# Kernel tuning notes

Hardware: AMD Instinct MI355X
Metric: run time of the kernel (lower is better)

The kernel has to match this reference:

```python
import jax, jax.numpy as jnp
import numpy as np

D = 768        # embed dim
DEPTH = 12     # num blocks
H = 12         # heads
HD = D // H    # head dim = 64
P = 16         # patch size
IMG = 224
NPATCH = (IMG // P) ** 2   # 196
N = NPATCH + 1             # +cls = 197
MLP = 4 * D                # 3072
NC = 100                   # classes
R = 8                      # lora rank
LORA_SCALE = 16.0 / R      # alpha / r = 2.0
EPS = 1e-6                 # timm LayerNorm eps


def setup_inputs() -> dict:
    key = jax.random.key(0)
    ks = jax.random.split(key, 12)
    def g(k, shape, s=0.02):
        return jax.random.normal(k, shape, dtype=jnp.float32) * s
    f32 = jnp.float32
    return {
        "x": jax.random.normal(ks[0], (32, 3, IMG, IMG), dtype=f32),
        "patch_w": g(ks[1], (D, 3, P, P)),
        "patch_b": jnp.zeros((D,), f32),
        "cls_token": g(ks[2], (1, 1, D)),
        "pos_embed": g(ks[3], (1, N, D)),
        "ln1_g": jnp.ones((DEPTH, D), f32),  "ln1_b": jnp.zeros((DEPTH, D), f32),
        "qkv_w": g(ks[4], (DEPTH, 3 * D, D)), "qkv_b": jnp.zeros((DEPTH, 3 * D), f32),
        "lora_A": g(ks[5], (DEPTH, D, R), 0.1), "lora_B": g(ks[6], (DEPTH, R, 3 * D), 0.1),
        "proj_w": g(ks[7], (DEPTH, D, D)), "proj_b": jnp.zeros((DEPTH, D), f32),
        "ln2_g": jnp.ones((DEPTH, D), f32),  "ln2_b": jnp.zeros((DEPTH, D), f32),
        "fc1_w": g(ks[8], (DEPTH, MLP, D)), "fc1_b": jnp.zeros((DEPTH, MLP), f32),
        "fc2_w": g(ks[9], (DEPTH, D, MLP)), "fc2_b": jnp.zeros((DEPTH, D), f32),
        "norm_g": jnp.ones((D,), f32), "norm_b": jnp.zeros((D,), f32),
        "head_w": g(ks[10], (NC, D)), "head_b": jnp.zeros((NC,), f32),
    }


def _ln(x, g, b):
    m = x.mean(-1, keepdims=True)
    v = ((x - m) ** 2).mean(-1, keepdims=True)
    return (x - m) * jax.lax.rsqrt(v + EPS) * g + b


def reference(x, patch_w, patch_b, cls_token, pos_embed,
              ln1_g, ln1_b, qkv_w, qkv_b, lora_A, lora_B, proj_w, proj_b,
              ln2_g, ln2_b, fc1_w, fc1_b, fc2_w, fc2_b,
              norm_g, norm_b, head_w, head_b):
    B = x.shape[0]
    # patch embed: non-overlapping PxP conv == unfold + linear
    xp = x.reshape(B, 3, IMG // P, P, IMG // P, P).transpose(0, 2, 4, 1, 3, 5)
    xp = xp.reshape(B, NPATCH, 3 * P * P)              # [B, 196, 768]
    t = xp @ patch_w.reshape(D, -1).T + patch_b        # [B, 196, D]
    t = jnp.concatenate([jnp.broadcast_to(cls_token, (B, 1, D)), t], axis=1)
    t = t + pos_embed                                   # [B, N, D]

    scale = HD ** -0.5
    for i in range(DEPTH):
        h = _ln(t, ln1_g[i], ln1_b[i])
        # frozen qkv GEMM + LoRA low-rank branch (dropout = identity at eval)
        qkv = h @ qkv_w[i].T + qkv_b[i] + ((h @ lora_A[i]) @ lora_B[i]) * LORA_SCALE
        qkv = qkv.reshape(B, N, 3, H, HD).transpose(2, 0, 3, 1, 4)  # [3, B, H, N, HD]
        q, k, v = qkv[0], qkv[1], qkv[2]
        attn = jax.nn.softmax(jnp.einsum('bhqd,bhkd->bhqk', q, k) * scale, axis=-1)
        o = jnp.einsum('bhqk,bhkd->bhqd', attn, v).transpose(0, 2, 1, 3).reshape(B, N, D)
        t = t + o @ proj_w[i].T + proj_b[i]
        h2 = _ln(t, ln2_g[i], ln2_b[i])
        t = t + jax.nn.gelu(h2 @ fc1_w[i].T + fc1_b[i], approximate=False) @ fc2_w[i].T + fc2_b[i]

    t = _ln(t, norm_g, norm_b)
    return t[:, 0] @ head_w.T + head_b  # cls-token pool -> head [B, NC]
```

## Files before the change

kernel.cpp:

```cpp
#include <hip/hip_runtime.h>

#define TOK  6304
#define MPAD 6400
#define NH   12
#define HD   64
#define BHD  384
#define NPD  256
#define QKVD 2304
#define PSTR 264

typedef float  f32x4  __attribute__((ext_vector_type(4)));
typedef __bf16 bf16x8 __attribute__((ext_vector_type(8)));

__device__ __forceinline__ unsigned short f2bf(float f) {
  unsigned u = __float_as_uint(f);
  return (unsigned short)((u + 0x7fffu + ((u >> 16) & 1u)) >> 16);
}
__device__ __forceinline__ float bf2f(unsigned short h) {
  return __uint_as_float(((unsigned)h) << 16);
}

__device__ __forceinline__ void gl2lds16(void* g, void* l) {
  __builtin_amdgcn_global_load_lds((__attribute__((address_space(1))) void*)g,
                                   (__attribute__((address_space(3))) void*)l, 16, 0, 0);
}

template<int BM, int BN, int MT, int NT, int WC>
__device__ __forceinline__ void gemm_core(const unsigned short* A, int lda,
                                          const unsigned short* B, int ldb,
                                          int K, int bm, int bn,
                                          unsigned short* lds,
                                          f32x4 (&acc)[MT][NT]) {
  const int tid  = threadIdx.x;
  const int wave = tid >> 6, lane = tid & 63;
  const int wr = wave / WC, wc = wave % WC;
  const int lh = lane >> 4, lm = lane & 15;
  unsigned short* ldsA = lds;
  unsigned short* ldsB = lds + BM * 32;
  constexpr int AIT = BM / 64, BIT = BN / 64;
  for (int k0 = 0; k0 < K; k0 += 32) {
    #pragma unroll
    for (int it = 0; it < AIT; ++it) {
      int idx16 = (wave * AIT + it) * 64 + lane;
      int row = idx16 >> 2, seg = idx16 & 3;
      gl2lds16((void*)(A + (long)(bm + row) * lda + k0 + seg * 8), ldsA + idx16 * 8);
    }
    #pragma unroll
    for (int it = 0; it < BIT; ++it) {
      int idx16 = (wave * BIT + it) * 64 + lane;
      int row = idx16 >> 2, seg = idx16 & 3;
      gl2lds16((void*)(B + (long)(bn + row) * ldb + k0 + seg * 8), ldsB + idx16 * 8);
    }
    __syncthreads();
    bf16x8 af[MT], bfr[NT];
    #pragma unroll
    for (int i = 0; i < MT; ++i)
      af[i] = *(const bf16x8*)(ldsA + (wr * MT * 16 + i * 16 + lm) * 32 + lh * 8);
    #pragma unroll
    for (int j = 0; j < NT; ++j)
      bfr[j] = *(const bf16x8*)(ldsB + (wc * NT * 16 + j * 16 + lm) * 32 + lh * 8);
    #pragma unroll
    for (int i = 0; i < MT; ++i)
      #pragma unroll
      for (int j = 0; j < NT; ++j)
        acc[i][j] = __builtin_amdgcn_mfma_f32_16x16x32_bf16(af[i], bfr[j], acc[i][j], 0, 0, 0);
    __syncthreads();
  }
}


__global__ __launch_bounds__(256) void k_cvt(const float4* __restrict__ s,
                                             ushort4* __restrict__ d, int n4) {
  int stride = gridDim.x * 256;
  for (int i = blockIdx.x * 256 + threadIdx.x; i < n4; i += stride) {
    float4 v = s[i];
    ushort4 o;
    o.x = f2bf(v.x); o.y = f2bf(v.y); o.z = f2bf(v.z); o.w = f2bf(v.w);
    d[i] = o;
  }
}

__global__ __launch_bounds__(256) void k_unfold(const float* __restrict__ x,
                                                unsigned short* __restrict__ xp) {
  int idx = blockIdx.x * 256 + threadIdx.x;
  if (idx >= 32 * 196 * 768) return;
  int f = idx % 768; int rest = idx / 768;
  int p = rest % 196; int b = rest / 196;
  int c = f >> 8, ij = f & 255, i = ij >> 4, j = ij & 15;
  int py = p / 14, px = p % 14;
  xp[idx] = f2bf(x[(((long)b * 3 + c) * 224 + py * 16 + i) * 224 + px * 16 + j]);
}

__global__ __launch_bounds__(256) void k_cls(const float* __restrict__ cls,
                                             const float* __restrict__ pos,
                                             float* __restrict__ t) {
  int i = blockIdx.x * 256 + threadIdx.x;
  int b = i / 768, d = i % 768;
  t[((long)(b * 197)) * 768 + d] = cls[d] + pos[d];
}

__global__ __launch_bounds__(256) void k_ln(const float* __restrict__ t,
                                            const float* __restrict__ gw,
                                            const float* __restrict__ bw,
                                            unsigned short* __restrict__ h,
                                            const float* __restrict__ A,
                                            float* __restrict__ hA) {
  __shared__ float red[4];
  __shared__ float red8[32];
  int row = blockIdx.x, tid = threadIdx.x;
  const float* x = t + (long)row * 768;
  float v0 = x[tid], v1 = x[tid + 256], v2 = x[tid + 512];
  float s = v0 + v1 + v2;
  #pragma unroll
  for (int off = 32; off > 0; off >>= 1) s += __shfl_xor(s, off, 64);
  int wave = tid >> 6, lane = tid & 63;
  if (lane == 0) red[wave] = s;
  __syncthreads();
  s = red[0] + red[1] + red[2] + red[3];
  float mean = s * (1.f / 768.f);
  float d0 = v0 - mean, d1 = v1 - mean, d2 = v2 - mean;
  float s2 = d0 * d0 + d1 * d1 + d2 * d2;
  __syncthreads();
  #pragma unroll
  for (int off = 32; off > 0; off >>= 1) s2 += __shfl_xor(s2, off, 64);
  if (lane == 0) red[wave] = s2;
  __syncthreads();
  s2 = red[0] + red[1] + red[2] + red[3];
  float rstd = rsqrtf(s2 * (1.f / 768.f) + 1e-6f);
  float n0 = d0 * rstd * gw[tid]       + bw[tid];
  float n1 = d1 * rstd * gw[tid + 256] + bw[tid + 256];
  float n2 = d2 * rstd * gw[tid + 512] + bw[tid + 512];
  unsigned short* hr = h + (long)row * 768;
  hr[tid]       = f2bf(n0);
  hr[tid + 256] = f2bf(n1);
  hr[tid + 512] = f2bf(n2);
  if (A) {
    float a[8];
    const float* A0 = A + (long)tid * 8;
    const float* A1 = A + (long)(tid + 256) * 8;
    const float* A2 = A + (long)(tid + 512) * 8;
    #pragma unroll
    for (int rr = 0; rr < 8; ++rr) a[rr] = n0 * A0[rr] + n1 * A1[rr] + n2 * A2[rr];
    #pragma unroll
    for (int rr = 0; rr < 8; ++rr) {
      #pragma unroll
      for (int off = 32; off > 0; off >>= 1) a[rr] += __shfl_xor(a[rr], off, 64);
    }
    if (lane == 0) {
      #pragma unroll
      for (int rr = 0; rr < 8; ++rr) red8[wave * 8 + rr] = a[rr];
    }
    __syncthreads();
    if (tid < 8) hA[(long)row * 8 + tid] = red8[tid] + red8[8 + tid] + red8[16 + tid] + red8[24 + tid];
  }
}

__global__ __launch_bounds__(256) void k_head(const float* __restrict__ t,
                                              const float* __restrict__ ng,
                                              const float* __restrict__ nb,
                                              const float* __restrict__ hw,
                                              const float* __restrict__ hb,
                                              float* __restrict__ out) {
  __shared__ float xs[768];
  __shared__ float red[4];
  int b = blockIdx.x, tid = threadIdx.x;
  const float* x = t + ((long)(b * 197)) * 768;
  float v0 = x[tid], v1 = x[tid + 256], v2 = x[tid + 512];
  float s = v0 + v1 + v2;
  #pragma unroll
  for (int off = 32; off > 0; off >>= 1) s += __shfl_xor(s, off, 64);
  int wave = tid >> 6, lane = tid & 63;
  if (lane == 0) red[wave] = s;
  __syncthreads();
  s = red[0] + red[1] + red[2] + red[3];
  float mean = s * (1.f / 768.f);
  float d0 = v0 - mean, d1 = v1 - mean, d2 = v2 - mean;
  float s2 = d0 * d0 + d1 * d1 + d2 * d2;
  __syncthreads();
  #pragma unroll
  for (int off = 32; off > 0; off >>= 1) s2 += __shfl_xor(s2, off, 64);
  if (lane == 0) red[wave] = s2;
  __syncthreads();
  s2 = red[0] + red[1] + red[2] + red[3];
  float rstd = rsqrtf(s2 * (1.f / 768.f) + 1e-6f);
  xs[tid]       = d0 * rstd * ng[tid]       + nb[tid];
  xs[tid + 256] = d1 * rstd * ng[tid + 256] + nb[tid + 256];
  xs[tid + 512] = d2 * rstd * ng[tid + 512] + nb[tid + 512];
  __syncthreads();
  for (int n = tid; n < 100; n += 256) {
    const float* wr = hw + (long)n * 768;
    float acc = hb[n];
    for (int k2 = 0; k2 < 768; ++k2) acc += xs[k2] * wr[k2];
    out[b * 100 + n] = acc;
  }
}


__global__ __launch_bounds__(256) void k_patch_gemm(
    const unsigned short* __restrict__ xp, const unsigned short* __restrict__ w,
    const float* __restrict__ bias, const float* __restrict__ pos,
    float* __restrict__ t) {
  __shared__ unsigned short lds[(128 + 128) * 32];
  f32x4 acc[4][4] = {};
  int bm = blockIdx.x * 128, bn = blockIdx.y * 128;
  gemm_core<128, 128, 4, 4, 2>(xp, 768, w, 768, 768, bm, bn, lds, acc);
  const int wave = threadIdx.x >> 6, lane = threadIdx.x & 63;
  const int wr = wave >> 1, wc = wave & 1, lh = lane >> 4, lm = lane & 15;
  #pragma unroll
  for (int i = 0; i < 4; ++i)
  #pragma unroll
  for (int r = 0; r < 4; ++r) {
    int m = bm + wr * 64 + i * 16 + lh * 4 + r;
    int b = m / 196, p = m % 196;
    long trow = ((long)(b * 197 + 1 + p)) * 768;
    #pragma unroll
    for (int j = 0; j < 4; ++j) {
      int n = bn + wc * 64 + j * 16 + lm;
      t[trow + n] = acc[i][j][r] + bias[n] + pos[(1 + p) * 768 + n];
    }
  }
}

__global__ __launch_bounds__(256) void k_qkv(
    const unsigned short* __restrict__ h, const unsigned short* __restrict__ w,
    const float* __restrict__ bias, const float* __restrict__ hA,
    const float* __restrict__ loraB,
    unsigned short* __restrict__ q, unsigned short* __restrict__ kk,
    unsigned short* __restrict__ vT) {
  __shared__ unsigned short lds[(128 + 128) * 32];
  f32x4 acc[4][4] = {};
  int bm = blockIdx.x * 128, bn = blockIdx.y * 128;
  gemm_core<128, 128, 4, 4, 2>(h, 768, w, 768, 768, bm, bn, lds, acc);
  const int wave = threadIdx.x >> 6, lane = threadIdx.x & 63;
  const int wr = wave >> 1, wc = wave & 1, lh = lane >> 4, lm = lane & 15;
  float lb[4][8];
  float bia[4];
  #pragma unroll
  for (int j = 0; j < 4; ++j) {
    int n = bn + wc * 64 + j * 16 + lm;
    bia[j] = bias[n];
    #pragma unroll
    for (int rr = 0; rr < 8; ++rr) lb[j][rr] = loraB[rr * QKVD + n];
  }
  #pragma unroll
  for (int i = 0; i < 4; ++i)
  #pragma unroll
  for (int r = 0; r < 4; ++r) {
    int m = bm + wr * 64 + i * 16 + lh * 4 + r;
    if (m >= TOK) continue;
    int b = m / 197, tok = m % 197;
    const float* ha = hA + (long)m * 8;
    float hv[8];
    #pragma unroll
    for (int rr = 0; rr < 8; ++rr) hv[rr] = ha[rr];
    #pragma unroll
    for (int j = 0; j < 4; ++j) {
      int n = bn + wc * 64 + j * 16 + lm;
      float lora = 0.f;
      #pragma unroll
      for (int rr = 0; rr < 8; ++rr) lora += hv[rr] * lb[j][rr];
      float v = acc[i][j][r] + bia[j] + 2.0f * lora;
      int which = n / 768;
      int nr = n - which * 768;
      int hh = nr >> 6, dd = nr & 63;
      long base = (long)(b * NH + hh);
      unsigned short bv = f2bf(v);
      if (which == 0)      q [(base * NPD + tok) * HD + dd] = bv;
      else if (which == 1) kk[(base * NPD + tok) * HD + dd] = bv;
      else                 vT[(base * HD + dd) * NPD + tok] = bv;
    }
  }
}

__global__ __launch_bounds__(256) void k_attn(
    const unsigned short* __restrict__ q, const unsigned short* __restrict__ kk,
    const unsigned short* __restrict__ vT, unsigned short* __restrict__ o) {
  __shared__ unsigned short lds[128 * PSTR + 64 * 32];
  f32x4 acc[2][16] = {};
  int bh = blockIdx.y;
  int bm = blockIdx.x * 128;
  gemm_core<128, 256, 2, 16, 1>(q + (long)bh * NPD * HD, HD,
                                kk + (long)bh * NPD * HD, HD, HD, bm, 0, lds, acc);
  const int tid = threadIdx.x, wave = tid >> 6, lane = tid & 63;
  const int lh = lane >> 4, lm = lane & 15;
  unsigned short* Plds = lds;
  #pragma unroll
  for (int i = 0; i < 2; ++i) {
    #pragma unroll
    for (int r = 0; r < 4; ++r) {
      float sv[16]; float mx = -3e38f;
      #pragma unroll
      for (int j = 0; j < 16; ++j) {
        float s = acc[i][j][r] * 0.125f;
        if (j * 16 + lm >= 197) s = -3e38f;
        sv[j] = s; mx = fmaxf(mx, s);
      }
      #pragma unroll
      for (int off = 1; off < 16; off <<= 1) mx = fmaxf(mx, __shfl_xor(mx, off, 64));
      float sum = 0.f;
      #pragma unroll
      for (int j = 0; j < 16; ++j) {
        float e = (sv[j] < -1e38f) ? 0.f : __expf(sv[j] - mx);
        sv[j] = e; sum += e;
      }
      #pragma unroll
      for (int off = 1; off < 16; off <<= 1) sum += __shfl_xor(sum, off, 64);
      float inv = 1.f / sum;
      int row = wave * 32 + i * 16 + lh * 4 + r;
      #pragma unroll
      for (int j = 0; j < 16; ++j) Plds[row * PSTR + j * 16 + lm] = f2bf(sv[j] * inv);
    }
  }
  f32x4 acc2[2][4] = {};
  const unsigned short* V = vT + (long)bh * HD * NPD;
  unsigned short* Vst = lds + 128 * PSTR;
  for (int k0 = 0; k0 < NPD; k0 += 32) {
    gl2lds16((void*)(V + (long)(tid >> 2) * NPD + k0 + (tid & 3) * 8), Vst + tid * 8);
    __syncthreads();
    bf16x8 af[2], bfr[4];
    #pragma unroll
    for (int i = 0; i < 2; ++i)
      af[i] = *(const bf16x8*)(Plds + (wave * 32 + i * 16 + lm) * PSTR + k0 + lh * 8);
    #pragma unroll
    for (int j = 0; j < 4; ++j)
      bfr[j] = *(const bf16x8*)(Vst + (j * 16 + lm) * 32 + lh * 8);
    #pragma unroll
    for (int i = 0; i < 2; ++i)
      #pragma unroll
      for (int j = 0; j < 4; ++j)
        acc2[i][j] = __builtin_amdgcn_mfma_f32_16x16x32_bf16(af[i], bfr[j], acc2[i][j], 0, 0, 0);
    __syncthreads();
  }
  int b = bh / NH, hh = bh % NH;
  #pragma unroll
  for (int i = 0; i < 2; ++i)
  #pragma unroll
  for (int r = 0; r < 4; ++r) {
    int m = bm + wave * 32 + i * 16 + lh * 4 + r;
    if (m >= 197) continue;
    long ob = ((long)(b * 197 + m)) * 768 + hh * 64;
    #pragma unroll
    for (int j = 0; j < 4; ++j) o[ob + j * 16 + lm] = f2bf(acc2[i][j][r]);
  }
}

__global__ __launch_bounds__(256) void k_proj(
    const unsigned short* __restrict__ o, const unsigned short* __restrict__ w,
    const float* __restrict__ bias, float* __restrict__ t) {
  __shared__ unsigned short lds[(128 + 128) * 32];
  f32x4 acc[4][4] = {};
  int bm = blockIdx.x * 128, bn = blockIdx.y * 128;
  gemm_core<128, 128, 4, 4, 2>(o, 768, w, 768, 768, bm, bn, lds, acc);
  const int wave = threadIdx.x >> 6, lane = threadIdx.x & 63;
  const int wr = wave >> 1, wc = wave & 1, lh = lane >> 4, lm = lane & 15;
  #pragma unroll
  for (int i = 0; i < 4; ++i)
  #pragma unroll
  for (int r = 0; r < 4; ++r) {
    int m = bm + wr * 64 + i * 16 + lh * 4 + r;
    if (m >= TOK) continue;
    long trow = (long)m * 768;
    #pragma unroll
    for (int j = 0; j < 4; ++j) {
      int n = bn + wc * 64 + j * 16 + lm;
      t[trow + n] = acc[i][j][r] + bias[n] + t[trow + n];
    }
  }
}

__global__ __launch_bounds__(256) void k_fc1(
    const unsigned short* __restrict__ h, const unsigned short* __restrict__ w,
    const float* __restrict__ bias, unsigned short* __restrict__ g) {
  __shared__ unsigned short lds[(128 + 128) * 32];
  f32x4 acc[4][4] = {};
  int bm = blockIdx.x * 128, bn = blockIdx.y * 128;
  gemm_core<128, 128, 4, 4, 2>(h, 768, w, 768, 768, bm, bn, lds, acc);
  const int wave = threadIdx.x >> 6, lane = threadIdx.x & 63;
  const int wr = wave >> 1, wc = wave & 1, lh = lane >> 4, lm = lane & 15;
  #pragma unroll
  for (int i = 0; i < 4; ++i)
  #pragma unroll
  for (int r = 0; r < 4; ++r) {
    int m = bm + wr * 64 + i * 16 + lh * 4 + r;
    if (m >= TOK) continue;
    long grow = (long)m * 3072;
    #pragma unroll
    for (int j = 0; j < 4; ++j) {
      int n = bn + wc * 64 + j * 16 + lm;
      float u = acc[i][j][r] + bias[n];
      float ge = 0.5f * u * (1.f + erff(u * 0.70710678118654752440f));
      g[grow + n] = f2bf(ge);
    }
  }
}

__global__ __launch_bounds__(256) void k_fc2(
    const unsigned short* __restrict__ g, const unsigned short* __restrict__ w,
    const float* __restrict__ bias, float* __restrict__ t) {
  __shared__ unsigned short lds[(128 + 128) * 32];
  f32x4 acc[4][4] = {};
  int bm = blockIdx.x * 128, bn = blockIdx.y * 128;
  gemm_core<128, 128, 4, 4, 2>(g, 3072, w, 3072, 3072, bm, bn, lds, acc);
  const int wave = threadIdx.x >> 6, lane = threadIdx.x & 63;
  const int wr = wave >> 1, wc = wave & 1, lh = lane >> 4, lm = lane & 15;
  #pragma unroll
  for (int i = 0; i < 4; ++i)
  #pragma unroll
  for (int r = 0; r < 4; ++r) {
    int m = bm + wr * 64 + i * 16 + lh * 4 + r;
    if (m >= TOK) continue;
    long trow = (long)m * 768;
    #pragma unroll
    for (int j = 0; j < 4; ++j) {
      int n = bn + wc * 64 + j * 16 + lm;
      t[trow + n] = acc[i][j][r] + bias[n] + t[trow + n];
    }
  }
}


extern "C" void kernel_launch(void* const* d_in, const int* in_sizes, int n_in,
                              void* d_out, int out_size, void* d_ws, size_t ws_size,
                              hipStream_t stream) {
  const float* x       = (const float*)d_in[0];
  const float* patch_w = (const float*)d_in[1];
  const float* patch_b = (const float*)d_in[2];
  const float* cls_tok = (const float*)d_in[3];
  const float* pos     = (const float*)d_in[4];
  const float* ln1_g   = (const float*)d_in[5];
  const float* ln1_b   = (const float*)d_in[6];
  const float* qkv_w   = (const float*)d_in[7];
  const float* qkv_b   = (const float*)d_in[8];
  const float* lora_A  = (const float*)d_in[9];
  const float* lora_B  = (const float*)d_in[10];
  const float* proj_w  = (const float*)d_in[11];
  const float* proj_b  = (const float*)d_in[12];
  const float* ln2_g   = (const float*)d_in[13];
  const float* ln2_b   = (const float*)d_in[14];
  const float* fc1_w   = (const float*)d_in[15];
  const float* fc1_b   = (const float*)d_in[16];
  const float* fc2_w   = (const float*)d_in[17];
  const float* fc2_b   = (const float*)d_in[18];
  const float* norm_g  = (const float*)d_in[19];
  const float* norm_b  = (const float*)d_in[20];
  const float* head_w  = (const float*)d_in[21];
  const float* head_b  = (const float*)d_in[22];
  float* out = (float*)d_out;
  (void)in_sizes; (void)n_in; (void)out_size;

  char* cur = (char*)d_ws;
  size_t used = 0;
  auto take = [&](size_t bytes) -> char* {
    char* r = cur;
    size_t pad = (bytes + 255) & ~(size_t)255;
    cur += pad; used += pad;
    return r;
  };
  unsigned short* xp  = (unsigned short*)take((size_t)6272 * 768 * 2);
  float*          t   = (float*)take((size_t)MPAD * 768 * 4);
  unsigned short* h   = (unsigned short*)take((size_t)MPAD * 768 * 2);
  float*          hA  = (float*)take((size_t)MPAD * 8 * 4);
  unsigned short* q   = (unsigned short*)take((size_t)BHD * NPD * HD * 2);
  unsigned short* kk  = (unsigned short*)take((size_t)BHD * NPD * HD * 2);
  unsigned short* vT  = (unsigned short*)take((size_t)BHD * NPD * HD * 2);
  unsigned short* o   = (unsigned short*)take((size_t)MPAD * 768 * 2);
  unsigned short* g   = (unsigned short*)take((size_t)MPAD * 3072 * 2);
  unsigned short* wpatch = (unsigned short*)take((size_t)768 * 768 * 2);

  const size_t EQKV = (size_t)12 * 2304 * 768, EPROJ = (size_t)12 * 768 * 768,
               EFC1 = (size_t)12 * 3072 * 768, EFC2 = (size_t)12 * 768 * 3072;
  size_t fullBytes = (EQKV + EPROJ + EFC1 + EFC2) * 2 + 4 * 256;
  bool full = (ws_size > used) && (ws_size - used >= fullBytes);
  unsigned short *wqkv = 0, *wproj = 0, *wfc1 = 0, *wfc2 = 0, *wbuf = 0;
  if (full) {
    wqkv  = (unsigned short*)take(EQKV * 2);
    wproj = (unsigned short*)take(EPROJ * 2);
    wfc1  = (unsigned short*)take(EFC1 * 2);
    wfc2  = (unsigned short*)take(EFC2 * 2);
  } else {
    wbuf  = (unsigned short*)take((size_t)3072 * 768 * 2);
  }

  auto cvt = [&](const float* src, unsigned short* dst, size_t n) {
    int n4 = (int)(n / 4);
    int grid = (n4 + 255) / 256; if (grid > 4096) grid = 4096;
    k_cvt<<<grid, 256, 0, stream>>>((const float4*)src, (ushort4*)dst, n4);
  };

  cvt(patch_w, wpatch, (size_t)768 * 768);
  if (full) {
    cvt(qkv_w,  wqkv,  EQKV);
    cvt(proj_w, wproj, EPROJ);
    cvt(fc1_w,  wfc1,  EFC1);
    cvt(fc2_w,  wfc2,  EFC2);
  }

  k_unfold<<<(32 * 196 * 768 + 255) / 256, 256, 0, stream>>>(x, xp);
  k_cls<<<(32 * 768) / 256, 256, 0, stream>>>(cls_tok, pos, t);
  k_patch_gemm<<<dim3(49, 6), 256, 0, stream>>>(xp, wpatch, patch_b, pos, t);

  for (int i = 0; i < 12; ++i) {
    k_ln<<<TOK, 256, 0, stream>>>(t, ln1_g + i * 768, ln1_b + i * 768, h,
                                  lora_A + (size_t)i * 768 * 8, hA);
    const unsigned short* wq;
    if (full) wq = wqkv + (size_t)i * 2304 * 768;
    else { cvt(qkv_w + (size_t)i * 2304 * 768, wbuf, (size_t)2304 * 768); wq = wbuf; }
    k_qkv<<<dim3(50, 18), 256, 0, stream>>>(h, wq, qkv_b + (size_t)i * 2304,
                                            hA, lora_B + (size_t)i * 8 * 2304, q, kk, vT);
    k_attn<<<dim3(2, BHD), 256, 0, stream>>>(q, kk, vT, o);
    const unsigned short* wp;
    if (full) wp = wproj + (size_t)i * 768 * 768;
    else { cvt(proj_w + (size_t)i * 768 * 768, wbuf, (size_t)768 * 768); wp = wbuf; }
    k_proj<<<dim3(50, 6), 256, 0, stream>>>(o, wp, proj_b + (size_t)i * 768, t);
    k_ln<<<TOK, 256, 0, stream>>>(t, ln2_g + i * 768, ln2_b + i * 768, h,
                                  (const float*)nullptr, (float*)nullptr);
    const unsigned short* w1;
    if (full) w1 = wfc1 + (size_t)i * 3072 * 768;
    else { cvt(fc1_w + (size_t)i * 3072 * 768, wbuf, (size_t)3072 * 768); w1 = wbuf; }
    k_fc1<<<dim3(50, 24), 256, 0, stream>>>(h, w1, fc1_b + (size_t)i * 3072, g);
    const unsigned short* w2;
    if (full) w2 = wfc2 + (size_t)i * 768 * 3072;
    else { cvt(fc2_w + (size_t)i * 768 * 3072, wbuf, (size_t)768 * 3072); w2 = wbuf; }
    k_fc2<<<dim3(50, 6), 256, 0, stream>>>(g, w2, fc2_b + (size_t)i * 768, t);
  }

  k_head<<<32, 256, 0, stream>>>(t, norm_g, norm_b, head_w, head_b, out);
}
```

Before: 4.024 ms.

## Use K=64 LDS tiles with XOR swizzle and smaller M tiles for proj/fc2

The shared GEMM core now stages 64-wide K slices per iteration instead of 32, halving the number of barrier pairs, and XOR-swizzles the 16-byte segments in LDS to avoid bank conflicts on fragment reads. The attention PV loop gets the same K=64 swizzled staging. The proj and fc2 GEMMs switch to 64-row M tiles with twice as many blocks so that the N=768 GEMMs fill more of the GPU. LDS use per block doubles, which may lower occupancy.

```diff
diff --git a/kernel.cpp b/kernel.cpp
--- a/kernel.cpp
+++ b/kernel.cpp
@@ -26,44 +26,51 @@
 }
 
 template<int BM, int BN, int MT, int NT, int WC>
-__device__ __forceinline__ void gemm_core(const unsigned short* A, int lda,
-                                          const unsigned short* B, int ldb,
-                                          int K, int bm, int bn,
-                                          unsigned short* lds,
-                                          f32x4 (&acc)[MT][NT]) {
+__device__ __forceinline__ void gemm64(const unsigned short* A, int lda,
+                                       const unsigned short* B, int ldb,
+                                       int K, int bm, int bn,
+                                       unsigned short* lds,
+                                       f32x4 (&acc)[MT][NT]) {
   const int tid  = threadIdx.x;
   const int wave = tid >> 6, lane = tid & 63;
   const int wr = wave / WC, wc = wave % WC;
   const int lh = lane >> 4, lm = lane & 15;
   unsigned short* ldsA = lds;
-  unsigned short* ldsB = lds + BM * 32;
-  constexpr int AIT = BM / 64, BIT = BN / 64;
-  for (int k0 = 0; k0 < K; k0 += 32) {
+  unsigned short* ldsB = lds + BM * 64;
+  constexpr int AIT = BM * 64 / 2048, BIT = BN * 64 / 2048;
+  for (int k0 = 0; k0 < K; k0 += 64) {
     #pragma unroll
     for (int it = 0; it < AIT; ++it) {
-      int idx16 = (wave * AIT + it) * 64 + lane;
-      int row = idx16 >> 2, seg = idx16 & 3;
-      gl2lds16((void*)(A + (long)(bm + row) * lda + k0 + seg * 8), ldsA + idx16 * 8);
+      int idx = (wave * AIT + it) * 64 + lane;
+      int row = idx >> 3, seg = (idx & 7) ^ (row & 7);
+      gl2lds16((void*)(A + (long)(bm + row) * lda + k0 + seg * 8), ldsA + idx * 8);
     }
     #pragma unroll
     for (int it = 0; it < BIT; ++it) {
-      int idx16 = (wave * BIT + it) * 64 + lane;
-      int row = idx16 >> 2, seg = idx16 & 3;
-      gl2lds16((void*)(B + (long)(bn + row) * ldb + k0 + seg * 8), ldsB + idx16 * 8);
+      int idx = (wave * BIT + it) * 64 + lane;
+      int row = idx >> 3, seg = (idx & 7) ^ (row & 7);
+      gl2lds16((void*)(B + (long)(bn + row) * ldb + k0 + seg * 8), ldsB + idx * 8);
     }
     __syncthreads();
-    bf16x8 af[MT], bfr[NT];
-    #pragma unroll
-    for (int i = 0; i < MT; ++i)
-      af[i] = *(const bf16x8*)(ldsA + (wr * MT * 16 + i * 16 + lm) * 32 + lh * 8);
-    #pragma unroll
-    for (int j = 0; j < NT; ++j)
-      bfr[j] = *(const bf16x8*)(ldsB + (wc * NT * 16 + j * 16 + lm) * 32 + lh * 8);
-    #pragma unroll
-    for (int i = 0; i < MT; ++i)
-      #pragma unroll
-      for (int j = 0; j < NT; ++j)
-        acc[i][j] = __builtin_amdgcn_mfma_f32_16x16x32_bf16(af[i], bfr[j], acc[i][j], 0, 0, 0);
+    #pragma unroll
+    for (int kk2 = 0; kk2 < 2; ++kk2) {
+      bf16x8 af[MT], bfr[NT];
+      #pragma unroll
+      for (int i = 0; i < MT; ++i) {
+        int ra = wr * MT * 16 + i * 16 + lm;
+        af[i] = *(const bf16x8*)(ldsA + ra * 64 + ((((kk2 << 2) | lh) ^ (ra & 7)) << 3));
+      }
+      #pragma unroll
+      for (int j = 0; j < NT; ++j) {
+        int rb = wc * NT * 16 + j * 16 + lm;
+        bfr[j] = *(const bf16x8*)(ldsB + rb * 64 + ((((kk2 << 2) | lh) ^ (rb & 7)) << 3));
+      }
+      #pragma unroll
+      for (int i = 0; i < MT; ++i)
+        #pragma unroll
+        for (int j = 0; j < NT; ++j)
+          acc[i][j] = __builtin_amdgcn_mfma_f32_16x16x32_bf16(af[i], bfr[j], acc[i][j], 0, 0, 0);
+    }
     __syncthreads();
   }
 }
@@ -200,10 +207,10 @@
     const unsigned short* __restrict__ xp, const unsigned short* __restrict__ w,
     const float* __restrict__ bias, const float* __restrict__ pos,
     float* __restrict__ t) {
-  __shared__ unsigned short lds[(128 + 128) * 32];
+  __shared__ unsigned short lds[(128 + 128) * 64];
   f32x4 acc[4][4] = {};
   int bm = blockIdx.x * 128, bn = blockIdx.y * 128;
-  gemm_core<128, 128, 4, 4, 2>(xp, 768, w, 768, 768, bm, bn, lds, acc);
+  gemm64<128, 128, 4, 4, 2>(xp, 768, w, 768, 768, bm, bn, lds, acc);
   const int wave = threadIdx.x >> 6, lane = threadIdx.x & 63;
   const int wr = wave >> 1, wc = wave & 1, lh = lane >> 4, lm = lane & 15;
   #pragma unroll
@@ -227,10 +234,10 @@
     const float* __restrict__ loraB,
     unsigned short* __restrict__ q, unsigned short* __restrict__ kk,
     unsigned short* __restrict__ vT) {
-  __shared__ unsigned short lds[(128 + 128) * 32];
+  __shared__ unsigned short lds[(128 + 128) * 64];
   f32x4 acc[4][4] = {};
   int bm = blockIdx.x * 128, bn = blockIdx.y * 128;
-  gemm_core<128, 128, 4, 4, 2>(h, 768, w, 768, 768, bm, bn, lds, acc);
+  gemm64<128, 128, 4, 4, 2>(h, 768, w, 768, 768, bm, bn, lds, acc);
   const int wave = threadIdx.x >> 6, lane = threadIdx.x & 63;
   const int wr = wave >> 1, wc = wave & 1, lh = lane >> 4, lm = lane & 15;
   float lb[4][8];
@@ -275,12 +282,12 @@
 __global__ __launch_bounds__(256) void k_attn(
     const unsigned short* __restrict__ q, const unsigned short* __restrict__ kk,
     const unsigned short* __restrict__ vT, unsigned short* __restrict__ o) {
-  __shared__ unsigned short lds[128 * PSTR + 64 * 32];
+  __shared__ unsigned short lds[128 * PSTR + 64 * 64];
   f32x4 acc[2][16] = {};
   int bh = blockIdx.y;
   int bm = blockIdx.x * 128;
-  gemm_core<128, 256, 2, 16, 1>(q + (long)bh * NPD * HD, HD,
-                                kk + (long)bh * NPD * HD, HD, HD, bm, 0, lds, acc);
+  gemm64<128, 256, 2, 16, 1>(q + (long)bh * NPD * HD, HD,
+                             kk + (long)bh * NPD * HD, HD, HD, bm, 0, lds, acc);
   const int tid = threadIdx.x, wave = tid >> 6, lane = tid & 63;
   const int lh = lane >> 4, lm = lane & 15;
   unsigned short* Plds = lds;
@@ -314,21 +321,31 @@
   f32x4 acc2[2][4] = {};
   const unsigned short* V = vT + (long)bh * HD * NPD;
   unsigned short* Vst = lds + 128 * PSTR;
-  for (int k0 = 0; k0 < NPD; k0 += 32) {
-    gl2lds16((void*)(V + (long)(tid >> 2) * NPD + k0 + (tid & 3) * 8), Vst + tid * 8);
+  for (int k0 = 0; k0 < NPD; k0 += 64) {
+    #pragma unroll
+    for (int it = 0; it < 2; ++it) {
+      int idx = (wave * 2 + it) * 64 + lane;
+      int row = idx >> 3, seg = (idx & 7) ^ (row & 7);
+      gl2lds16((void*)(V + (long)row * NPD + k0 + seg * 8), Vst + idx * 8);
+    }
     __syncthreads();
-    bf16x8 af[2], bfr[4];
-    #pragma unroll
-    for (int i = 0; i < 2; ++i)
-      af[i] = *(const bf16x8*)(Plds + (wave * 32 + i * 16 + lm) * PSTR + k0 + lh * 8);
-    #pragma unroll
-    for (int j = 0; j < 4; ++j)
-      bfr[j] = *(const bf16x8*)(Vst + (j * 16 + lm) * 32 + lh * 8);
-    #pragma unroll
-    for (int i = 0; i < 2; ++i)
-      #pragma unroll
-      for (int j = 0; j < 4; ++j)
-        acc2[i][j] = __builtin_amdgcn_mfma_f32_16x16x32_bf16(af[i], bfr[j], acc2[i][j], 0, 0, 0);
+    #pragma unroll
+    for (int kk2 = 0; kk2 < 2; ++kk2) {
+      bf16x8 af[2], bfr[4];
+      #pragma unroll
+      for (int i = 0; i < 2; ++i)
+        af[i] = *(const bf16x8*)(Plds + (wave * 32 + i * 16 + lm) * PSTR + k0 + kk2 * 32 + lh * 8);
+      #pragma unroll
+      for (int j = 0; j < 4; ++j) {
+        int rv = j * 16 + lm;
+        bfr[j] = *(const bf16x8*)(Vst + rv * 64 + ((((kk2 << 2) | lh) ^ (rv & 7)) << 3));
+      }
+      #pragma unroll
+      for (int i = 0; i < 2; ++i)
+        #pragma unroll
+        for (int j = 0; j < 4; ++j)
+          acc2[i][j] = __builtin_amdgcn_mfma_f32_16x16x32_bf16(af[i], bfr[j], acc2[i][j], 0, 0, 0);
+    }
     __syncthreads();
   }
   int b = bh / NH, hh = bh % NH;
@@ -347,17 +364,17 @@
 __global__ __launch_bounds__(256) void k_proj(
     const unsigned short* __restrict__ o, const unsigned short* __restrict__ w,
     const float* __restrict__ bias, float* __restrict__ t) {
-  __shared__ unsigned short lds[(128 + 128) * 32];
-  f32x4 acc[4][4] = {};
-  int bm = blockIdx.x * 128, bn = blockIdx.y * 128;
-  gemm_core<128, 128, 4, 4, 2>(o, 768, w, 768, 768, bm, bn, lds, acc);
+  __shared__ unsigned short lds[(64 + 128) * 64];
+  f32x4 acc[2][4] = {};
+  int bm = blockIdx.x * 64, bn = blockIdx.y * 128;
+  gemm64<64, 128, 2, 4, 2>(o, 768, w, 768, 768, bm, bn, lds, acc);
   const int wave = threadIdx.x >> 6, lane = threadIdx.x & 63;
   const int wr = wave >> 1, wc = wave & 1, lh = lane >> 4, lm = lane & 15;
   #pragma unroll
-  for (int i = 0; i < 4; ++i)
+  for (int i = 0; i < 2; ++i)
   #pragma unroll
   for (int r = 0; r < 4; ++r) {
-    int m = bm + wr * 64 + i * 16 + lh * 4 + r;
+    int m = bm + wr * 32 + i * 16 + lh * 4 + r;
     if (m >= TOK) continue;
     long trow = (long)m * 768;
     #pragma unroll
@@ -371,10 +388,10 @@
 __global__ __launch_bounds__(256) void k_fc1(
     const unsigned short* __restrict__ h, const unsigned short* __restrict__ w,
     const float* __restrict__ bias, unsigned short* __restrict__ g) {
-  __shared__ unsigned short lds[(128 + 128) * 32];
+  __shared__ unsigned short lds[(128 + 128) * 64];
   f32x4 acc[4][4] = {};
   int bm = blockIdx.x * 128, bn = blockIdx.y * 128;
-  gemm_core<128, 128, 4, 4, 2>(h, 768, w, 768, 768, bm, bn, lds, acc);
+  gemm64<128, 128, 4, 4, 2>(h, 768, w, 768, 768, bm, bn, lds, acc);
   const int wave = threadIdx.x >> 6, lane = threadIdx.x & 63;
   const int wr = wave >> 1, wc = wave & 1, lh = lane >> 4, lm = lane & 15;
   #pragma unroll
@@ -397,17 +414,17 @@
 __global__ __launch_bounds__(256) void k_fc2(
     const unsigned short* __restrict__ g, const unsigned short* __restrict__ w,
     const float* __restrict__ bias, float* __restrict__ t) {
-  __shared__ unsigned short lds[(128 + 128) * 32];
-  f32x4 acc[4][4] = {};
-  int bm = blockIdx.x * 128, bn = blockIdx.y * 128;
-  gemm_core<128, 128, 4, 4, 2>(g, 3072, w, 3072, 3072, bm, bn, lds, acc);
+  __shared__ unsigned short lds[(64 + 128) * 64];
+  f32x4 acc[2][4] = {};
+  int bm = blockIdx.x * 64, bn = blockIdx.y * 128;
+  gemm64<64, 128, 2, 4, 2>(g, 3072, w, 3072, 3072, bm, bn, lds, acc);
   const int wave = threadIdx.x >> 6, lane = threadIdx.x & 63;
   const int wr = wave >> 1, wc = wave & 1, lh = lane >> 4, lm = lane & 15;
   #pragma unroll
-  for (int i = 0; i < 4; ++i)
+  for (int i = 0; i < 2; ++i)
   #pragma unroll
   for (int r = 0; r < 4; ++r) {
-    int m = bm + wr * 64 + i * 16 + lh * 4 + r;
+    int m = bm + wr * 32 + i * 16 + lh * 4 + r;
     if (m >= TOK) continue;
     long trow = (long)m * 768;
     #pragma unroll
@@ -511,7 +528,7 @@
     const unsigned short* wp;
     if (full) wp = wproj + (size_t)i * 768 * 768;
     else { cvt(proj_w + (size_t)i * 768 * 768, wbuf, (size_t)768 * 768); wp = wbuf; }
-    k_proj<<<dim3(50, 6), 256, 0, stream>>>(o, wp, proj_b + (size_t)i * 768, t);
+    k_proj<<<dim3(100, 6), 256, 0, stream>>>(o, wp, proj_b + (size_t)i * 768, t);
     k_ln<<<TOK, 256, 0, stream>>>(t, ln2_g + i * 768, ln2_b + i * 768, h,
                                   (const float*)nullptr, (float*)nullptr);
     const unsigned short* w1;
@@ -521,7 +538,7 @@
     const unsigned short* w2;
     if (full) w2 = wfc2 + (size_t)i * 768 * 3072;
     else { cvt(fc2_w + (size_t)i * 768 * 3072, wbuf, (size_t)768 * 3072); w2 = wbuf; }
-    k_fc2<<<dim3(50, 6), 256, 0, stream>>>(g, w2, fc2_b + (size_t)i * 768, t);
+    k_fc2<<<dim3(100, 6), 256, 0, stream>>>(g, w2, fc2_b + (size_t)i * 768, t);
   }
 
   k_head<<<32, 256, 0, stream>>>(t, norm_g, norm_b, head_w, head_b, out);
```

After: 3.910 ms. 2.8% less time.
